# Optimization experiments

Hardware: AMD Instinct MI355X
Metric: run time of the kernel (lower is better)

Reference implementation:

```python
import jax, jax.numpy as jnp
import numpy as np

K_PER_CLASS = 10
WINDOW = 7
MIN_MASS = 0.05
EPS = 1e-8


def _pool_sum(x, w):
    # sum-pool over last two dims, stride 1, zero padding w//2 (count_include_pad avg = sum / w^2)
    nd = x.ndim
    return jax.lax.reduce_window(
        x, 0.0, jax.lax.add,
        (1,) * (nd - 2) + (w, w),
        (1,) * nd,
        [(0, 0)] * (nd - 2) + [(w // 2, w // 2)] * 2,
    )


def _l2norm(x, axis):
    # matches torch F.normalize(p=2): x / max(||x||, 1e-12)
    return x / jnp.maximum(jnp.linalg.norm(x, axis=axis, keepdims=True), 1e-12)


def setup_inputs() -> dict:
    key = jax.random.key(0)
    k1, k2, k3 = jax.random.split(key, 3)
    feature_map = jax.random.normal(k1, (8, 512, 96, 96), dtype=jnp.float32)
    prototypes = jax.random.normal(k2, (80, 512), dtype=jnp.float32)
    pseudo_mask = jax.random.randint(k3, (8, 96, 96), 0, 9, dtype=jnp.int32)
    return {"feature_map": feature_map, "prototypes": prototypes, "pseudo_mask": pseudo_mask}


def reference(feature_map, prototypes, pseudo_mask):
    B, D, H, W = feature_map.shape
    K = K_PER_CLASS
    C = prototypes.shape[0] // K
    area = WINDOW * WINDOW

    Fn = _l2norm(feature_map, 1)                       # [B,D,H,W]
    Pn = _l2norm(prototypes, 1).reshape(C, K, D)       # [C,K,D]
    sim = jnp.einsum('bdhw,ckd->bckhw', Fn, Pn)        # [B,C,K,H,W]

    omega = (pseudo_mask[:, None] == (jnp.arange(C) + 1)[None, :, None, None]).astype(sim.dtype)  # [B,C,H,W]

    num = _pool_sum(sim * omega[:, :, None], WINDOW) / area   # [B,C,K,H,W]
    den = _pool_sum(omega, WINDOW) / area                      # [B,C,H,W]
    region = num / (den[:, :, None] + EPS)

    a = region.reshape(B, C, K, H * W).transpose(0, 1, 3, 2)   # [B,C,HW,K]
    valid = (den > MIN_MASS).reshape(B, C, H * W)
    V = valid.sum(-1)                                          # [B,C] int
    Vf = jnp.maximum(V, 1).astype(a.dtype)
    vm = valid[..., None].astype(a.dtype)

    mean = (a * vm).sum(2) / Vf[..., None]                     # [B,C,K]
    a_c = (a - mean[:, :, None]) * vm                          # zero out invalid rows
    nrm = jnp.sqrt((a_c * a_c).sum(2))                         # [B,C,K]
    a_n = a_c / (nrm[:, :, None] + EPS)

    gram = jnp.einsum('bcvk,bcvl->bckl', a_n, a_n) / Vf[..., None, None]  # [B,C,K,K]
    off = gram * (1.0 - jnp.eye(K, dtype=gram.dtype))
    loss_c = (off * off).sum((-1, -2)) / (K * (K - 1))         # [B,C]

    active = (omega.sum((-1, -2)) >= 1.0) & (V >= 2)           # mirrors skip conditions
    af = active.astype(loss_c.dtype)
    per_image = (loss_c * af).sum(-1) / jnp.maximum(af.sum(-1), 1.0)
    return per_image.sum() / B
```

## Files before the change

kernel.cpp:

```cpp
#include <hip/hip_runtime.h>
#include <cstdint>
#include <cstddef>

namespace {
constexpr int Bn = 8, Dn = 512, Hn = 96, Wn = 96, HWn = Hn * Wn;
constexpr int Cn = 8, Kn = 10, CKn = Cn * Kn;
constexpr int NPIX = Bn * HWn;
constexpr int NCHUNK = 4, DCH = Dn / NCHUNK;
constexpr int NMOM = 66;
constexpr float EPSF = 1e-8f;
constexpr float MINM = 0.05f;

constexpr size_t oPnT  = 0;
constexpr size_t oS    = oPnT + (size_t)Dn * CKn;
constexpr size_t oNumH = oS + (size_t)Bn * Kn * HWn;
constexpr size_t oPart = oNumH;
constexpr size_t oDenH = oNumH + (size_t)Bn * Cn * Kn * HWn;
constexpr size_t oMom  = oDenH + (size_t)Bn * Cn * HWn;
constexpr size_t oCnt  = oMom + 64 * NMOM;
constexpr size_t oEnd  = oCnt + 64;
}

__device__ __forceinline__ float wred64(float v) {
#pragma unroll
    for (int o = 32; o > 0; o >>= 1) v += __shfl_down(v, o, 64);
    return v;
}

__global__ __launch_bounds__(64) void k_protonorm(const float* __restrict__ P,
                                                  float* __restrict__ PnT) {
    int ck = blockIdx.x, lane = threadIdx.x;
    float v[8]; float ss = 0.f;
#pragma unroll
    for (int j = 0; j < 8; ++j) { v[j] = P[ck * Dn + lane + 64 * j]; ss += v[j] * v[j]; }
    ss = wred64(ss);
    ss = __shfl(ss, 0, 64);
    float inv = 1.0f / fmaxf(sqrtf(ss), 1e-12f);
#pragma unroll
    for (int j = 0; j < 8; ++j)
        PnT[(size_t)(lane + 64 * j) * CKn + ck] = v[j] * inv;
}

__global__ __launch_bounds__(256) void k_sim(const float* __restrict__ F,
                                             const float* __restrict__ PnT,
                                             const int* __restrict__ mask,
                                             float* __restrict__ part) {
    __shared__ float pch[64 * 96];
    const int tid = threadIdx.x;
    const int pix = blockIdx.x * 256 + tid;
    const int chunk = blockIdx.y;
    const int b = pix / HWn, hw = pix % HWn;

    const int m = mask[pix];
    const int cc = m > 0 ? m - 1 : 0;

    float acc[Kn]; float ss = 0.f;
#pragma unroll
    for (int k = 0; k < Kn; ++k) acc[k] = 0.f;

    for (int p = 0; p < DCH / 64; ++p) {
        const int dbase = chunk * DCH + p * 64;
        __syncthreads();
        for (int i = tid; i < 64 * CKn; i += 256) {
            int dd = i / CKn, ck = i % CKn;
            int c = ck / Kn, kk = ck % Kn;
            pch[dd * 96 + c * 12 + kk] = PnT[(size_t)(dbase + dd) * CKn + ck];
        }
        __syncthreads();
#pragma unroll 4
        for (int dd = 0; dd < 64; ++dd) {
            float f = F[(size_t)(b * Dn + dbase + dd) * HWn + hw];
            ss += f * f;
            const float4* p4 = (const float4*)&pch[dd * 96 + cc * 12];
            float4 pa = p4[0], pb = p4[1];
            float2 pc = *(const float2*)&pch[dd * 96 + cc * 12 + 8];
            acc[0] += f * pa.x; acc[1] += f * pa.y; acc[2] += f * pa.z; acc[3] += f * pa.w;
            acc[4] += f * pb.x; acc[5] += f * pb.y; acc[6] += f * pb.z; acc[7] += f * pb.w;
            acc[8] += f * pc.x; acc[9] += f * pc.y;
        }
    }
#pragma unroll
    for (int k = 0; k < Kn; ++k)
        part[(size_t)(chunk * 11 + k) * NPIX + pix] = acc[k];
    part[(size_t)(chunk * 11 + 10) * NPIX + pix] = ss;
}

__global__ __launch_bounds__(256) void k_simred(const float* __restrict__ part,
                                                const int* __restrict__ mask,
                                                float* __restrict__ S,
                                                int* __restrict__ cnt) {
    __shared__ int hist[Cn];
    const int tid = threadIdx.x;
    const int pix = blockIdx.x * 256 + tid;
    if (tid < Cn) hist[tid] = 0;
    __syncthreads();

    float acc[Kn]; float ss = 0.f;
#pragma unroll
    for (int k = 0; k < Kn; ++k) acc[k] = 0.f;
#pragma unroll
    for (int ch = 0; ch < NCHUNK; ++ch) {
#pragma unroll
        for (int k = 0; k < Kn; ++k)
            acc[k] += part[(size_t)(ch * 11 + k) * NPIX + pix];
        ss += part[(size_t)(ch * 11 + 10) * NPIX + pix];
    }
    float inv = 1.0f / fmaxf(sqrtf(ss), 1e-12f);
    const int b = pix / HWn, hw = pix % HWn;
#pragma unroll
    for (int k = 0; k < Kn; ++k)
        S[(size_t)(b * Kn + k) * HWn + hw] = acc[k] * inv;

    const int m = mask[pix];
    if (m > 0) atomicAdd(&hist[m - 1], 1);
    __syncthreads();
    if (tid < Cn) atomicAdd(&cnt[(pix / HWn) * Cn + tid], hist[tid]);
}

__global__ __launch_bounds__(256) void k_hpool(const int* __restrict__ mask,
                                               const float* __restrict__ S,
                                               float* __restrict__ numH,
                                               float* __restrict__ denH) {
    const int t = blockIdx.x * 256 + threadIdx.x;
    const int wg = t % 24;
    int r = t / 24;
    const int h = r % Hn; r /= Hn;
    const int k2 = r % 5;
    const int bc = r / 5;
    const int c = bc & 7, b = bc >> 3;
    const int k0 = 2 * k2;
    const int w0 = wg * 4;
    const int rowb = b * HWn + h * Wn;
    const float* S0 = &S[(size_t)(b * Kn + k0) * HWn + h * Wn];
    const float* S1 = &S[(size_t)(b * Kn + k0 + 1) * HWn + h * Wn];

    float a0[4] = {0.f, 0.f, 0.f, 0.f};
    float a1[4] = {0.f, 0.f, 0.f, 0.f};
    float dn[4] = {0.f, 0.f, 0.f, 0.f};

#pragma unroll
    for (int dc = -3; dc <= 6; ++dc) {
        int ww = w0 + dc;
        if (ww < 0 || ww >= Wn) continue;
        float hv = (mask[rowb + ww] == c + 1) ? 1.0f : 0.0f;
        float s0 = S0[ww] * hv;
        float s1 = S1[ww] * hv;
        const int olo = dc - 3 > 0 ? dc - 3 : 0;
        const int ohi = dc + 3 < 3 ? dc + 3 : 3;
#pragma unroll
        for (int o = 0; o < 4; ++o) {
            if (o < olo || o > ohi) continue;
            a0[o] += s0; a1[o] += s1; dn[o] += hv;
        }
    }
    float4* n0 = (float4*)&numH[(size_t)(bc * Kn + k0) * HWn + h * Wn + w0];
    float4* n1 = (float4*)&numH[(size_t)(bc * Kn + k0 + 1) * HWn + h * Wn + w0];
    *n0 = make_float4(a0[0], a0[1], a0[2], a0[3]);
    *n1 = make_float4(a1[0], a1[1], a1[2], a1[3]);
    if (k2 == 0)
        *(float4*)&denH[(size_t)bc * HWn + h * Wn + w0] =
            make_float4(dn[0], dn[1], dn[2], dn[3]);
}

__global__ __launch_bounds__(256) void k_vpool(const float* __restrict__ numH,
                                               const float* __restrict__ denH,
                                               float* __restrict__ mom) {
    const int t = blockIdx.x * 256 + threadIdx.x;
    const int w = t % Wn;
    int r = t / Wn;
    const int hg = r % 24;
    const int bc = r / 24;
    const int h0 = hg * 4;

    float nacc[4][Kn];
    float dacc[4] = {0.f, 0.f, 0.f, 0.f};
#pragma unroll
    for (int o = 0; o < 4; ++o)
#pragma unroll
        for (int k = 0; k < Kn; ++k) nacc[o][k] = 0.f;

#pragma unroll
    for (int dr = -3; dr <= 6; ++dr) {
        int hh = h0 + dr;
        if (hh < 0 || hh >= Hn) continue;
        const int olo = dr - 3 > 0 ? dr - 3 : 0;
        const int ohi = dr + 3 < 3 ? dr + 3 : 3;
        float dv = denH[(size_t)bc * HWn + hh * Wn + w];
#pragma unroll
        for (int o = 0; o < 4; ++o) {
            if (o < olo || o > ohi) continue;
            dacc[o] += dv;
        }
#pragma unroll
        for (int k = 0; k < Kn; ++k) {
            float nv = numH[(size_t)(bc * Kn + k) * HWn + hh * Wn + w];
#pragma unroll
            for (int o = 0; o < 4; ++o) {
                if (o < olo || o > ohi) continue;
                nacc[o][k] += nv;
            }
        }
    }

    float m[NMOM];
#pragma unroll
    for (int i = 0; i < NMOM; ++i) m[i] = 0.f;
#pragma unroll
    for (int o = 0; o < 4; ++o) {
        float dA = dacc[o] * (1.0f / 49.0f);
        float inv = 1.0f / (dA + EPSF);
        float vm = (dA > MINM) ? 1.0f : 0.0f;
        float rr[Kn];
#pragma unroll
        for (int k = 0; k < Kn; ++k)
            rr[k] = nacc[o][k] * (1.0f / 49.0f) * inv * vm;
        m[0] += vm;
#pragma unroll
        for (int k = 0; k < Kn; ++k) m[1 + k] += rr[k];
        int p = 11;
#pragma unroll
        for (int k = 0; k < Kn; ++k)
#pragma unroll
            for (int l = 0; l <= k; ++l, ++p) m[p] += rr[k] * rr[l];
    }

    __shared__ float red[4][NMOM];
    const int lane = threadIdx.x & 63, wv = threadIdx.x >> 6;
#pragma unroll
    for (int i = 0; i < NMOM; ++i) {
        float x = wred64(m[i]);
        if (lane == 0) red[wv][i] = x;
    }
    __syncthreads();
    for (int i = threadIdx.x; i < NMOM; i += 256)
        atomicAdd(&mom[bc * NMOM + i],
                  red[0][i] + red[1][i] + red[2][i] + red[3][i]);
}

__global__ __launch_bounds__(64) void k_final(const float* __restrict__ mom,
                                              const int* __restrict__ cnt,
                                              float* __restrict__ out) {
    const int bc = threadIdx.x;
    float mo[NMOM];
#pragma unroll
    for (int i = 0; i < NMOM; ++i) mo[i] = mom[bc * NMOM + i];
    const float V = mo[0];
    const float Vf = fmaxf(V, 1.0f);
    float Sk[Kn];
#pragma unroll
    for (int k = 0; k < Kn; ++k) Sk[k] = mo[1 + k];

    float M[55];
    {
        int p = 0;
#pragma unroll
        for (int k = 0; k < Kn; ++k)
#pragma unroll
            for (int l = 0; l <= k; ++l, ++p)
                M[p] = mo[11 + p] - Sk[k] * Sk[l] / Vf;
    }
    float nrm[Kn];
#pragma unroll
    for (int k = 0; k < Kn; ++k)
        nrm[k] = sqrtf(fmaxf(M[k * (k + 1) / 2 + k], 0.0f));
    float loss = 0.f;
    {
        int p = 0;
#pragma unroll
        for (int k = 0; k < Kn; ++k) {
#pragma unroll
            for (int l = 0; l <= k; ++l, ++p) {
                if (l == k) continue;
                float g = M[p] / ((nrm[k] + EPSF) * (nrm[l] + EPSF)) / Vf;
                loss += 2.0f * g * g;
            }
        }
    }
    loss *= 1.0f / (float)(Kn * (Kn - 1));
    bool act = (cnt[bc] >= 1) && (V >= 2.0f);
    float sl = act ? loss : 0.f;
    float sa = act ? 1.f : 0.f;
#pragma unroll
    for (int o = 4; o > 0; o >>= 1) {
        sl += __shfl_down(sl, o, 8);
        sa += __shfl_down(sa, o, 8);
    }
    __shared__ float pimg[Bn];
    if ((bc & 7) == 0) pimg[bc >> 3] = sl / fmaxf(sa, 1.0f);
    __syncthreads();
    if (bc == 0) {
        float tot = 0.f;
#pragma unroll
        for (int b = 0; b < Bn; ++b) tot += pimg[b];
        out[0] = tot / (float)Bn;
    }
}

extern "C" void kernel_launch(void* const* d_in, const int* in_sizes, int n_in,
                              void* d_out, int out_size, void* d_ws, size_t ws_size,
                              hipStream_t stream) {
    const float* F  = (const float*)d_in[0];
    const float* P  = (const float*)d_in[1];
    const int* mask = (const int*)d_in[2];
    float* ws = (float*)d_ws;
    float* out = (float*)d_out;

    hipMemsetAsync(ws + oMom, 0, (oEnd - oMom) * sizeof(float), stream);

    k_protonorm<<<CKn, 64, 0, stream>>>(P, ws + oPnT);
    k_sim<<<dim3(NPIX / 256, NCHUNK), 256, 0, stream>>>(F, ws + oPnT, mask, ws + oPart);
    k_simred<<<NPIX / 256, 256, 0, stream>>>(ws + oPart, mask, ws + oS, (int*)(ws + oCnt));
    k_hpool<<<Bn * Cn * 5 * Hn * 24 / 256, 256, 0, stream>>>(mask, ws + oS,
                                                             ws + oNumH, ws + oDenH);
    k_vpool<<<Bn * Cn * 24 * Wn / 256, 256, 0, stream>>>(ws + oNumH, ws + oDenH, ws + oMom);
    k_final<<<1, 64, 0, stream>>>(ws + oMom, (const int*)(ws + oCnt), out);
}
```

Measured before the change: 285.6 us.

## Fuse horizontal and vertical pooling into one tiled kernel using shared memory

Merges the separate horizontal-pool and vertical-pool kernels into a single kernel. Each block handles an 8-row tile of one (batch, class) pair: it computes horizontal sums for the tile plus a 3-row halo into LDS, then does the vertical sums and moment accumulation from LDS. This removes the global round trip of the large numH/denH intermediates (about 6M floats written and read). In exchange it recomputes the horizontal sums for halo rows (14 rows per 8-row tile) and uses about 59KB of LDS per block, which may limit occupancy.

```diff
diff --git a/kernel.cpp b/kernel.cpp
--- a/kernel.cpp
+++ b/kernel.cpp
@@ -10,13 +10,12 @@
 constexpr int NMOM = 66;
 constexpr float EPSF = 1e-8f;
 constexpr float MINM = 0.05f;
+constexpr int HT = 8, HROWS = HT + 6, NTILE = Hn / HT;
 
 constexpr size_t oPnT  = 0;
 constexpr size_t oS    = oPnT + (size_t)Dn * CKn;
-constexpr size_t oNumH = oS + (size_t)Bn * Kn * HWn;
-constexpr size_t oPart = oNumH;
-constexpr size_t oDenH = oNumH + (size_t)Bn * Cn * Kn * HWn;
-constexpr size_t oMom  = oDenH + (size_t)Bn * Cn * HWn;
+constexpr size_t oPart = oS + (size_t)Bn * Kn * HWn;
+constexpr size_t oMom  = oPart + (size_t)NCHUNK * 11 * NPIX;
 constexpr size_t oCnt  = oMom + 64 * NMOM;
 constexpr size_t oEnd  = oCnt + 64;
 }
@@ -45,7 +44,7 @@
                                              const float* __restrict__ PnT,
                                              const int* __restrict__ mask,
                                              float* __restrict__ part) {
-    __shared__ float pch[64 * 96];
+    __shared__ alignas(16) float pch[64 * 96];
     const int tid = threadIdx.x;
     const int pix = blockIdx.x * 256 + tid;
     const int chunk = blockIdx.y;
@@ -117,103 +116,92 @@
     if (tid < Cn) atomicAdd(&cnt[(pix / HWn) * Cn + tid], hist[tid]);
 }
 
-__global__ __launch_bounds__(256) void k_hpool(const int* __restrict__ mask,
-                                               const float* __restrict__ S,
-                                               float* __restrict__ numH,
-                                               float* __restrict__ denH) {
-    const int t = blockIdx.x * 256 + threadIdx.x;
-    const int wg = t % 24;
-    int r = t / 24;
-    const int h = r % Hn; r /= Hn;
-    const int k2 = r % 5;
-    const int bc = r / 5;
+__global__ __launch_bounds__(256) void k_pool(const int* __restrict__ mask,
+                                              const float* __restrict__ S,
+                                              float* __restrict__ mom) {
+    __shared__ alignas(16) float hp[Kn][HROWS][Wn];
+    __shared__ alignas(16) float hd[HROWS][Wn];
+    __shared__ alignas(16) float red[4][NMOM];
+
+    const int tid = threadIdx.x;
+    const int ht = blockIdx.x % NTILE;
+    const int bc = blockIdx.x / NTILE;
     const int c = bc & 7, b = bc >> 3;
-    const int k0 = 2 * k2;
-    const int w0 = wg * 4;
-    const int rowb = b * HWn + h * Wn;
-    const float* S0 = &S[(size_t)(b * Kn + k0) * HWn + h * Wn];
-    const float* S1 = &S[(size_t)(b * Kn + k0 + 1) * HWn + h * Wn];
-
-    float a0[4] = {0.f, 0.f, 0.f, 0.f};
-    float a1[4] = {0.f, 0.f, 0.f, 0.f};
-    float dn[4] = {0.f, 0.f, 0.f, 0.f};
-
-#pragma unroll
-    for (int dc = -3; dc <= 6; ++dc) {
-        int ww = w0 + dc;
-        if (ww < 0 || ww >= Wn) continue;
-        float hv = (mask[rowb + ww] == c + 1) ? 1.0f : 0.0f;
-        float s0 = S0[ww] * hv;
-        float s1 = S1[ww] * hv;
-        const int olo = dc - 3 > 0 ? dc - 3 : 0;
-        const int ohi = dc + 3 < 3 ? dc + 3 : 3;
-#pragma unroll
-        for (int o = 0; o < 4; ++o) {
-            if (o < olo || o > ohi) continue;
-            a0[o] += s0; a1[o] += s1; dn[o] += hv;
-        }
-    }
-    float4* n0 = (float4*)&numH[(size_t)(bc * Kn + k0) * HWn + h * Wn + w0];
-    float4* n1 = (float4*)&numH[(size_t)(bc * Kn + k0 + 1) * HWn + h * Wn + w0];
-    *n0 = make_float4(a0[0], a0[1], a0[2], a0[3]);
-    *n1 = make_float4(a1[0], a1[1], a1[2], a1[3]);
-    if (k2 == 0)
-        *(float4*)&denH[(size_t)bc * HWn + h * Wn + w0] =
-            make_float4(dn[0], dn[1], dn[2], dn[3]);
-}
-
-__global__ __launch_bounds__(256) void k_vpool(const float* __restrict__ numH,
-                                               const float* __restrict__ denH,
-                                               float* __restrict__ mom) {
-    const int t = blockIdx.x * 256 + threadIdx.x;
-    const int w = t % Wn;
-    int r = t / Wn;
-    const int hg = r % 24;
-    const int bc = r / 24;
-    const int h0 = hg * 4;
-
-    float nacc[4][Kn];
-    float dacc[4] = {0.f, 0.f, 0.f, 0.f};
-#pragma unroll
-    for (int o = 0; o < 4; ++o)
-#pragma unroll
-        for (int k = 0; k < Kn; ++k) nacc[o][k] = 0.f;
-
-#pragma unroll
-    for (int dr = -3; dr <= 6; ++dr) {
-        int hh = h0 + dr;
+    const int h0 = ht * HT;
+
+    for (int u = tid; u < 5 * HROWS * 24; u += 256) {
+        const int wg = u % 24;
+        int r = u / 24;
+        const int row = r % HROWS;
+        const int k2 = r / HROWS;
+        const int hh = h0 - 3 + row;
         if (hh < 0 || hh >= Hn) continue;
-        const int olo = dr - 3 > 0 ? dr - 3 : 0;
-        const int ohi = dr + 3 < 3 ? dr + 3 : 3;
-        float dv = denH[(size_t)bc * HWn + hh * Wn + w];
-#pragma unroll
-        for (int o = 0; o < 4; ++o) {
-            if (o < olo || o > ohi) continue;
-            dacc[o] += dv;
-        }
-#pragma unroll
-        for (int k = 0; k < Kn; ++k) {
-            float nv = numH[(size_t)(bc * Kn + k) * HWn + hh * Wn + w];
+        const int k0 = 2 * k2;
+        const int w0 = wg * 4;
+        const int rowb = b * HWn + hh * Wn;
+        const float* S0 = &S[(size_t)(b * Kn + k0) * HWn + hh * Wn];
+        const float* S1 = S0 + HWn;
+
+        float a0[4] = {0.f, 0.f, 0.f, 0.f};
+        float a1[4] = {0.f, 0.f, 0.f, 0.f};
+        float dn[4] = {0.f, 0.f, 0.f, 0.f};
+#pragma unroll
+        for (int dc = -3; dc <= 6; ++dc) {
+            int ww = w0 + dc;
+            if (ww < 0 || ww >= Wn) continue;
+            float hv = (mask[rowb + ww] == c + 1) ? 1.0f : 0.0f;
+            float s0 = S0[ww] * hv;
+            float s1 = S1[ww] * hv;
+            const int olo = dc - 3 > 0 ? dc - 3 : 0;
+            const int ohi = dc + 3 < 3 ? dc + 3 : 3;
 #pragma unroll
             for (int o = 0; o < 4; ++o) {
                 if (o < olo || o > ohi) continue;
-                nacc[o][k] += nv;
+                a0[o] += s0; a1[o] += s1; dn[o] += hv;
             }
         }
-    }
+#pragma unroll
+        for (int o = 0; o < 4; ++o) {
+            hp[k0][row][w0 + o]     = a0[o];
+            hp[k0 + 1][row][w0 + o] = a1[o];
+        }
+        if (k2 == 0) {
+#pragma unroll
+            for (int o = 0; o < 4; ++o) hd[row][w0 + o] = dn[o];
+        }
+    }
+    __syncthreads();
 
     float m[NMOM];
 #pragma unroll
     for (int i = 0; i < NMOM; ++i) m[i] = 0.f;
-#pragma unroll
-    for (int o = 0; o < 4; ++o) {
-        float dA = dacc[o] * (1.0f / 49.0f);
-        float inv = 1.0f / (dA + EPSF);
-        float vm = (dA > MINM) ? 1.0f : 0.0f;
+
+    for (int idx = tid; idx < HT * Wn; idx += 256) {
+        const int w = idx % Wn;
+        const int oh = idx / Wn;
+        const int h = h0 + oh;
+
+        float dacc = 0.f;
+        float nacc[Kn];
+#pragma unroll
+        for (int k = 0; k < Kn; ++k) nacc[k] = 0.f;
+#pragma unroll
+        for (int dr = -3; dr <= 3; ++dr) {
+            const int hh = h + dr;
+            if (hh < 0 || hh >= Hn) continue;
+            const int row = hh - h0 + 3;
+            dacc += hd[row][w];
+#pragma unroll
+            for (int k = 0; k < Kn; ++k) nacc[k] += hp[k][row][w];
+        }
+
+        const float dA = dacc * (1.0f / 49.0f);
+        const float inv = 1.0f / (dA + EPSF);
+        const float vm = (dA > MINM) ? 1.0f : 0.0f;
         float rr[Kn];
 #pragma unroll
         for (int k = 0; k < Kn; ++k)
-            rr[k] = nacc[o][k] * (1.0f / 49.0f) * inv * vm;
+            rr[k] = nacc[k] * (1.0f / 49.0f) * inv * vm;
         m[0] += vm;
 #pragma unroll
         for (int k = 0; k < Kn; ++k) m[1 + k] += rr[k];
@@ -224,15 +212,14 @@
             for (int l = 0; l <= k; ++l, ++p) m[p] += rr[k] * rr[l];
     }
 
-    __shared__ float red[4][NMOM];
-    const int lane = threadIdx.x & 63, wv = threadIdx.x >> 6;
+    const int lane = tid & 63, wv = tid >> 6;
 #pragma unroll
     for (int i = 0; i < NMOM; ++i) {
         float x = wred64(m[i]);
         if (lane == 0) red[wv][i] = x;
     }
     __syncthreads();
-    for (int i = threadIdx.x; i < NMOM; i += 256)
+    for (int i = tid; i < NMOM; i += 256)
         atomicAdd(&mom[bc * NMOM + i],
                   red[0][i] + red[1][i] + red[2][i] + red[3][i]);
 }
@@ -310,8 +297,6 @@
     k_protonorm<<<CKn, 64, 0, stream>>>(P, ws + oPnT);
     k_sim<<<dim3(NPIX / 256, NCHUNK), 256, 0, stream>>>(F, ws + oPnT, mask, ws + oPart);
     k_simred<<<NPIX / 256, 256, 0, stream>>>(ws + oPart, mask, ws + oS, (int*)(ws + oCnt));
-    k_hpool<<<Bn * Cn * 5 * Hn * 24 / 256, 256, 0, stream>>>(mask, ws + oS,
-                                                             ws + oNumH, ws + oDenH);
-    k_vpool<<<Bn * Cn * 24 * Wn / 256, 256, 0, stream>>>(ws + oNumH, ws + oDenH, ws + oMom);
+    k_pool<<<64 * NTILE, 256, 0, stream>>>(mask, ws + oS, ws + oMom);
     k_final<<<1, 64, 0, stream>>>(ws + oMom, (const int*)(ws + oCnt), out);
 }
```

After: 294.4 us. +3.1%, slower.
